# Kernel tuning notes

Hardware: AMD Instinct MI355X
Metric: run time of the kernel (lower is better)

The kernel has to match this reference:

```python
import jax, jax.numpy as jnp
import numpy as np

B, M, L, LQ, E, V = 32, 100, 30, 30, 256, 32000


def position_encoding(seq_len, emb):
    # faithful to MemN2N position encoding: 1 + 4*(k - (E+1)/2)*(j - (J+1)/2)/(E*J)
    j = jnp.arange(1, seq_len + 1, dtype=jnp.float32)[:, None]   # (J,1)
    k = jnp.arange(1, emb + 1, dtype=jnp.float32)[None, :]       # (1,E)
    half_e = (emb + 1) / 2.0
    half_j = (seq_len + 1) / 2.0
    return 1.0 + 4.0 * (k - half_e) * (j - half_j) / (emb * seq_len)  # (J,E)


def masked_softmax(x, m):
    xm = jnp.where(m > 0, x, -1e30)
    e = jnp.exp(xm - jnp.max(xm, axis=-1, keepdims=True)) * m
    return e / (jnp.sum(e, axis=-1, keepdims=True) + 1e-13)


def masked_log_softmax(x, m):
    return jax.nn.log_softmax(x + jnp.log(m + 1e-13), axis=-1)


def _forward(trainS, trainQ, trainVM, trainPM, trainSM, trainQM,
             A1, A2, A3, A4, W, b, gamma, beta):
    # query encoding: embed + position encode + query mask + sum over words
    Q = trainQ[:, 0, :]                                   # (B,LQ)
    pe_q = position_encoding(LQ, E)                       # (LQ,E)
    u = jnp.sum(A1[Q] * pe_q * trainQM[:, :, None], axis=1)  # (B,E)

    # story memory embeddings: gather + PE + sum over words.
    # NOTE: original code multiplies by trainSM but discards the result (bug),
    # so SM is intentionally NOT applied here.
    pe_s = position_encoding(L, E)                        # (L,E)
    embA1 = jnp.sum(A1[trainS] * pe_s, axis=2)            # (B,M,E)
    embA2 = jnp.sum(A2[trainS] * pe_s, axis=2)
    embA3 = jnp.sum(A3[trainS] * pe_s, axis=2)
    embA4 = jnp.sum(A4[trainS] * pe_s, axis=2)

    def hop(memA, memC, u):
        # scores = sum_E(memA * u) * PM (PM applied pre-sum is equivalent)
        scores = jnp.einsum('bme,be->bm', memA, u) * trainPM
        p = masked_softmax(scores, trainPM)               # (B,M)
        o = jnp.einsum('bm,bme->be', p, memC)             # (B,E)
        return o + u

    u = hop(embA1, embA2, u)   # hop 1
    u = hop(embA2, embA3, u)   # hop 2
    u = hop(embA3, embA4, u)   # hop 3

    # final linear + BatchNorm1d (training-mode batch stats, eps=1e-5)
    wx = u @ W.T + b                                      # (B,V)
    mean = jnp.mean(wx, axis=0)
    var = jnp.mean((wx - mean) ** 2, axis=0)
    y = gamma * (wx - mean) / jnp.sqrt(var + 1e-5) + beta
    return masked_log_softmax(y, trainVM)


def setup_inputs() -> dict:
    key = jax.random.key(0)
    ks = jax.random.split(key, 8)
    inp = {
        'trainS': jax.random.randint(ks[0], (B, M, L), 0, V, dtype=jnp.int32),
        'trainQ': jax.random.randint(ks[1], (B, 1, LQ), 0, V, dtype=jnp.int32),
        'trainVM': jnp.ones((B, V), jnp.float32),
        'trainPM': jnp.ones((B, M), jnp.float32),
        'trainSM': jnp.ones((B, M, L), jnp.float32),
        'trainQM': jnp.ones((B, LQ), jnp.float32),
        'A1': 0.1 * jax.random.normal(ks[2], (V, E), jnp.float32),
        'A2': 0.1 * jax.random.normal(ks[3], (V, E), jnp.float32),
        'A3': 0.1 * jax.random.normal(ks[4], (V, E), jnp.float32),
        'A4': 0.1 * jax.random.normal(ks[5], (V, E), jnp.float32),
        'W': jax.random.normal(ks[6], (V, E), jnp.float32) / np.sqrt(E),
        'b': jnp.zeros((V,), jnp.float32),
        'gamma': jnp.ones((V,), jnp.float32),
        'beta': jnp.zeros((V,), jnp.float32),
        'inspect': 0,
    }
    return inp


def reference(trainS, trainQ, trainVM, trainPM, trainSM, trainQM,
              A1, A2, A3, A4, W, b, gamma, beta, inspect):
    return _forward(trainS, trainQ, trainVM, trainPM, trainSM, trainQM,
                    A1, A2, A3, A4, W, b, gamma, beta)
```

## Files before the change

kernel.cpp:

```cpp
#include <hip/hip_runtime.h>
#include <math.h>

static constexpr int B_ = 32, M_ = 100, L_ = 30, LQ_ = 30, E_ = 256, V_ = 32000;

__global__ __launch_bounds__(256) void k_embed(const int* __restrict__ trainS,
                                               const float* __restrict__ A1,
                                               const float* __restrict__ A2,
                                               const float* __restrict__ A3,
                                               const float* __restrict__ A4,
                                               float* __restrict__ embA) {
    const int bm = blockIdx.x;
    const int tbl = threadIdx.x >> 6;
    const int e0 = (threadIdx.x & 63) * 4;
    const float* __restrict__ A = (tbl == 0) ? A1 : (tbl == 1) ? A2 : (tbl == 2) ? A3 : A4;
    const float half_e = (E_ + 1) * 0.5f;
    const float half_j = (L_ + 1) * 0.5f;
    const float inv = 1.0f / (float)(E_ * L_);
    const float k0 = (float)(e0 + 1) - half_e;
    const float k1 = k0 + 1.f, k2 = k0 + 2.f, k3 = k0 + 3.f;

    int idx[L_];
#pragma unroll
    for (int l = 0; l < L_; ++l) idx[l] = trainS[bm * L_ + l];

    float4 acc = make_float4(0.f, 0.f, 0.f, 0.f);
#pragma unroll
    for (int c = 0; c < 2; ++c) {
        float4 r[15];
#pragma unroll
        for (int j = 0; j < 15; ++j)
            r[j] = *reinterpret_cast<const float4*>(A + (size_t)idx[c * 15 + j] * E_ + e0);
        __builtin_amdgcn_sched_barrier(0);
#pragma unroll
        for (int j = 0; j < 15; ++j) {
            const int l = c * 15 + j;
            const float coef = 4.0f * ((float)(l + 1) - half_j) * inv;
            acc.x += r[j].x * (1.0f + coef * k0);
            acc.y += r[j].y * (1.0f + coef * k1);
            acc.z += r[j].z * (1.0f + coef * k2);
            acc.w += r[j].w * (1.0f + coef * k3);
        }
    }
    *reinterpret_cast<float4*>(embA + (size_t)tbl * (B_ * M_ * E_) + (size_t)bm * E_ + e0) = acc;
}

__global__ __launch_bounds__(1024) void k_hops(const int* __restrict__ trainQ,
                                               const float* __restrict__ trainQM,
                                               const float* __restrict__ A1,
                                               const float* __restrict__ embA,
                                               const float* __restrict__ trainPM,
                                               float* __restrict__ u_T,
                                               float* __restrict__ partial) {
    const int b = blockIdx.x;
    const int tid = threadIdx.x;
    const int lane = tid & 63;
    const int wave = tid >> 6;
    const int g = tid >> 8;
    const int e = tid & 255;
    if (tid == 0) partial[b] = 0.f;
    __shared__ float u_sh[E_];
    __shared__ float sc[M_];
    __shared__ float p_sh[M_];
    __shared__ float osum[4][E_];

    {
        const float half_e = (E_ + 1) * 0.5f;
        const float half_j = (LQ_ + 1) * 0.5f;
        const float inv = 1.0f / (float)(E_ * LQ_);
        const float ke = (float)(e + 1) - half_e;
        const int l0 = g * 8;
        const int ln = (LQ_ - l0 < 8) ? (LQ_ - l0) : 8;
        int qi[8];
        float qm[8];
#pragma unroll
        for (int j = 0; j < 8; ++j) {
            if (j < ln) {
                qi[j] = trainQ[b * LQ_ + l0 + j];
                qm[j] = trainQM[b * LQ_ + l0 + j];
            } else { qi[j] = 0; qm[j] = 0.f; }
        }
        float r[8];
#pragma unroll
        for (int j = 0; j < 8; ++j)
            r[j] = (j < ln) ? A1[(size_t)qi[j] * E_ + e] : 0.f;
        float part = 0.f;
#pragma unroll
        for (int j = 0; j < 8; ++j) {
            const float pe = 1.0f + 4.0f * ke * ((float)(l0 + j + 1) - half_j) * inv;
            part += r[j] * pe * qm[j];
        }
        osum[g][e] = part;
    }
    __syncthreads();
    if (tid < E_) u_sh[tid] = osum[0][tid] + osum[1][tid] + osum[2][tid] + osum[3][tid];
    __syncthreads();

    for (int hop = 0; hop < 3; ++hop) {
        const float* memA = embA + (size_t)hop * (B_ * M_ * E_) + (size_t)b * M_ * E_;
        const float* memC = memA + (size_t)(B_ * M_ * E_);
#pragma unroll 2
        for (int m = wave; m < M_; m += 16) {
            const float* row = memA + m * E_;
            float part = 0.f;
#pragma unroll
            for (int j = 0; j < 4; ++j)
                part += row[lane + 64 * j] * u_sh[lane + 64 * j];
#pragma unroll
            for (int off = 32; off > 0; off >>= 1)
                part += __shfl_xor(part, off, 64);
            if (lane == 0) sc[m] = part * trainPM[b * M_ + m];
        }
        __syncthreads();
        if (wave == 0) {
            const float pm0 = (lane < M_) ? trainPM[b * M_ + lane] : 0.f;
            const float pm1 = (lane + 64 < M_) ? trainPM[b * M_ + lane + 64] : 0.f;
            const float x0 = (lane < M_ && pm0 > 0.f) ? sc[lane] : -1e30f;
            const float x1 = (lane + 64 < M_ && pm1 > 0.f) ? sc[lane + 64] : -1e30f;
            float mx = fmaxf(x0, x1);
#pragma unroll
            for (int off = 32; off > 0; off >>= 1)
                mx = fmaxf(mx, __shfl_xor(mx, off, 64));
            const float e0v = (lane < M_) ? expf(x0 - mx) * pm0 : 0.f;
            const float e1v = (lane + 64 < M_) ? expf(x1 - mx) * pm1 : 0.f;
            float ssum = e0v + e1v;
#pragma unroll
            for (int off = 32; off > 0; off >>= 1)
                ssum += __shfl_xor(ssum, off, 64);
            const float invs = 1.0f / (ssum + 1e-13f);
            if (lane < M_) p_sh[lane] = e0v * invs;
            if (lane + 64 < M_) p_sh[lane + 64] = e1v * invs;
        }
        __syncthreads();
        {
            float acc = 0.f;
            const float* crow = memC + e;
            const int m0 = g * 25;
#pragma unroll 5
            for (int mm = 0; mm < 25; ++mm)
                acc += p_sh[m0 + mm] * crow[(size_t)(m0 + mm) * E_];
            osum[g][e] = acc;
        }
        __syncthreads();
        if (tid < E_) u_sh[tid] += osum[0][tid] + osum[1][tid] + osum[2][tid] + osum[3][tid];
        __syncthreads();
    }
    if (tid < E_) u_T[tid * B_ + b] = u_sh[tid];
}

__global__ __launch_bounds__(256) void k_output(const float* __restrict__ u_T,
                                                const float* __restrict__ Wm,
                                                const float* __restrict__ bias,
                                                const float* __restrict__ gamma,
                                                const float* __restrict__ beta,
                                                const float* __restrict__ VM,
                                                float* __restrict__ z,
                                                float* __restrict__ partial) {
    __shared__ float u_lds[E_ * B_];
    __shared__ float pex[B_];
    const int tid = threadIdx.x;
    for (int i = tid; i < (E_ * B_) / 4; i += 256)
        reinterpret_cast<float4*>(u_lds)[i] = reinterpret_cast<const float4*>(u_T)[i];
    if (tid < B_) pex[tid] = 0.f;
    __syncthreads();

    const int bg = tid & 7;
    const int vl = tid >> 3;
    const int v0 = blockIdx.x * 64 + vl * 2;
    const int v1 = v0 + 1;
    const float* __restrict__ wr0 = Wm + (size_t)v0 * E_;
    const float* __restrict__ wr1 = Wm + (size_t)v1 * E_;

    float accA[4] = {0.f, 0.f, 0.f, 0.f};
    float accB[4] = {0.f, 0.f, 0.f, 0.f};

#pragma unroll
    for (int c = 0; c < 8; ++c) {
        float4 wa[8], wb[8];
#pragma unroll
        for (int j = 0; j < 8; ++j) {
            wa[j] = reinterpret_cast<const float4*>(wr0)[c * 8 + j];
            wb[j] = reinterpret_cast<const float4*>(wr1)[c * 8 + j];
        }
        __builtin_amdgcn_sched_barrier(0);
#pragma unroll
        for (int j = 0; j < 8; ++j) {
#pragma unroll
            for (int eo = 0; eo < 4; ++eo) {
                const int e = c * 32 + j * 4 + eo;
                const float4 u4 = *reinterpret_cast<const float4*>(u_lds + e * B_ + bg * 4);
                const float w0 = (eo == 0) ? wa[j].x : (eo == 1) ? wa[j].y : (eo == 2) ? wa[j].z : wa[j].w;
                const float w1 = (eo == 0) ? wb[j].x : (eo == 1) ? wb[j].y : (eo == 2) ? wb[j].z : wb[j].w;
                accA[0] += w0 * u4.x; accA[1] += w0 * u4.y; accA[2] += w0 * u4.z; accA[3] += w0 * u4.w;
                accB[0] += w1 * u4.x; accB[1] += w1 * u4.y; accB[2] += w1 * u4.z; accB[3] += w1 * u4.w;
            }
        }
    }

    const float bvA = bias[v0], bvB = bias[v1];
    float s1a = 0.f, s2a = 0.f, s1b = 0.f, s2b = 0.f;
#pragma unroll
    for (int i = 0; i < 4; ++i) {
        accA[i] += bvA; accB[i] += bvB;
        s1a += accA[i]; s2a += accA[i] * accA[i];
        s1b += accB[i]; s2b += accB[i] * accB[i];
    }
#pragma unroll
    for (int off = 1; off < 8; off <<= 1) {
        s1a += __shfl_xor(s1a, off, 64);
        s2a += __shfl_xor(s2a, off, 64);
        s1b += __shfl_xor(s1b, off, 64);
        s2b += __shfl_xor(s2b, off, 64);
    }
    const float meanA = s1a * (1.0f / B_);
    const float meanB = s1b * (1.0f / B_);
    const float varA = s2a * (1.0f / B_) - meanA * meanA;
    const float varB = s2b * (1.0f / B_) - meanB * meanB;
    const float rstdA = rsqrtf(varA + 1e-5f);
    const float rstdB = rsqrtf(varB + 1e-5f);
    const float gA = gamma[v0], beA = beta[v0];
    const float gB = gamma[v1], beB = beta[v1];

    float exs[4];
#pragma unroll
    for (int i = 0; i < 4; ++i) {
        const int b = bg * 4 + i;
        const size_t row = (size_t)b * V_;
        const float vm0 = VM[row + v0] + 1e-13f;
        const float vm1 = VM[row + v1] + 1e-13f;
        const float y0 = gA * (accA[i] - meanA) * rstdA + beA;
        const float y1 = gB * (accB[i] - meanB) * rstdB + beB;
        z[row + v0] = y0 + logf(vm0);
        z[row + v1] = y1 + logf(vm1);
        exs[i] = vm0 * expf(y0) + vm1 * expf(y1);
    }
#pragma unroll
    for (int i = 0; i < 4; ++i)
        atomicAdd(&pex[bg * 4 + i], exs[i]);
    __syncthreads();
    if (tid < B_) atomicAdd(&partial[tid], pex[tid]);
}

__global__ __launch_bounds__(256) void k_final(const float* __restrict__ z,
                                               const float* __restrict__ partial,
                                               float* __restrict__ out) {
    const int idx = blockIdx.x * 256 + threadIdx.x;
    const int b = idx / (V_ / 4);
    const int v4 = idx % (V_ / 4);
    const float lse = logf(partial[b]);
    const float4 x = reinterpret_cast<const float4*>(z + (size_t)b * V_)[v4];
    float4 o;
    o.x = x.x - lse; o.y = x.y - lse; o.z = x.z - lse; o.w = x.w - lse;
    reinterpret_cast<float4*>(out + (size_t)b * V_)[v4] = o;
}

extern "C" void kernel_launch(void* const* d_in, const int* in_sizes, int n_in,
                              void* d_out, int out_size, void* d_ws, size_t ws_size,
                              hipStream_t stream) {
    const int* trainS = (const int*)d_in[0];
    const int* trainQ = (const int*)d_in[1];
    const float* trainVM = (const float*)d_in[2];
    const float* trainPM = (const float*)d_in[3];
    const float* trainQM = (const float*)d_in[5];
    const float* A1 = (const float*)d_in[6];
    const float* A2 = (const float*)d_in[7];
    const float* A3 = (const float*)d_in[8];
    const float* A4 = (const float*)d_in[9];
    const float* Wm = (const float*)d_in[10];
    const float* bias = (const float*)d_in[11];
    const float* gamma = (const float*)d_in[12];
    const float* beta = (const float*)d_in[13];
    float* out = (float*)d_out;

    float* ws = (float*)d_ws;
    float* u_T = ws;
    float* embA = ws + 8192;
    float* z = embA + 4 * (B_ * M_ * E_);
    float* partial = z + (size_t)B_ * V_;

    k_embed<<<B_ * M_, 256, 0, stream>>>(trainS, A1, A2, A3, A4, embA);
    k_hops<<<B_, 1024, 0, stream>>>(trainQ, trainQM, A1, embA, trainPM, u_T, partial);
    k_output<<<V_ / 64, 256, 0, stream>>>(u_T, Wm, bias, gamma, beta, trainVM, z, partial);
    k_final<<<(B_ * V_ / 4) / 256, 256, 0, stream>>>(z, partial, out);
}
```

Baseline: 107.0 us.

## Halve vocab rows per block, double-buffer W loads, shard softmax partial sums

The output GEMM kernel now gives each thread one vocab row instead of two and launches twice as many blocks. A non-unrolled loop double-buffers the W register loads so the next chunk is fetched while the current one is multiplied. The per-batch exp-sum accumulator is split into 8 slots indexed by block, which cuts global atomic contention, and the final kernel sums the slots. The intent is more parallelism and less register pressure, at the cost of more blocks each reloading the 32 KB u tile into LDS and halved reuse of each u value loaded from LDS.

```diff
diff --git a/kernel.cpp b/kernel.cpp
--- a/kernel.cpp
+++ b/kernel.cpp
@@ -57,7 +57,7 @@
     const int wave = tid >> 6;
     const int g = tid >> 8;
     const int e = tid & 255;
-    if (tid == 0) partial[b] = 0.f;
+    if (tid < 8) partial[b * 8 + tid] = 0.f;
     __shared__ float u_sh[E_];
     __shared__ float sc[M_];
     __shared__ float p_sh[M_];
@@ -165,79 +165,79 @@
 
     const int bg = tid & 7;
     const int vl = tid >> 3;
-    const int v0 = blockIdx.x * 64 + vl * 2;
-    const int v1 = v0 + 1;
-    const float* __restrict__ wr0 = Wm + (size_t)v0 * E_;
-    const float* __restrict__ wr1 = Wm + (size_t)v1 * E_;
-
-    float accA[4] = {0.f, 0.f, 0.f, 0.f};
-    float accB[4] = {0.f, 0.f, 0.f, 0.f};
-
-#pragma unroll
-    for (int c = 0; c < 8; ++c) {
-        float4 wa[8], wb[8];
-#pragma unroll
-        for (int j = 0; j < 8; ++j) {
-            wa[j] = reinterpret_cast<const float4*>(wr0)[c * 8 + j];
-            wb[j] = reinterpret_cast<const float4*>(wr1)[c * 8 + j];
-        }
-        __builtin_amdgcn_sched_barrier(0);
-#pragma unroll
-        for (int j = 0; j < 8; ++j) {
-#pragma unroll
-            for (int eo = 0; eo < 4; ++eo) {
-                const int e = c * 32 + j * 4 + eo;
-                const float4 u4 = *reinterpret_cast<const float4*>(u_lds + e * B_ + bg * 4);
-                const float w0 = (eo == 0) ? wa[j].x : (eo == 1) ? wa[j].y : (eo == 2) ? wa[j].z : wa[j].w;
-                const float w1 = (eo == 0) ? wb[j].x : (eo == 1) ? wb[j].y : (eo == 2) ? wb[j].z : wb[j].w;
-                accA[0] += w0 * u4.x; accA[1] += w0 * u4.y; accA[2] += w0 * u4.z; accA[3] += w0 * u4.w;
-                accB[0] += w1 * u4.x; accB[1] += w1 * u4.y; accB[2] += w1 * u4.z; accB[3] += w1 * u4.w;
+    const int v = blockIdx.x * 32 + vl;
+    const float* __restrict__ wr = Wm + (size_t)v * E_;
+
+    float acc[4] = {0.f, 0.f, 0.f, 0.f};
+    float4 wA[4], wB[4];
+#pragma unroll
+    for (int c = 0; c < 4; ++c) wA[c] = reinterpret_cast<const float4*>(wr)[c];
+
+#pragma unroll 1
+    for (int cc = 0; cc < 16; cc += 2) {
+#pragma unroll
+        for (int c = 0; c < 4; ++c) wB[c] = reinterpret_cast<const float4*>(wr)[(cc + 1) * 4 + c];
+#pragma unroll
+        for (int c = 0; c < 4; ++c) {
+#pragma unroll
+            for (int q = 0; q < 4; ++q) {
+                const int e = cc * 16 + c * 4 + q;
+                const float4 u4 = *reinterpret_cast<const float4*>(&u_lds[e * B_ + bg * 4]);
+                const float w = (q == 0) ? wA[c].x : (q == 1) ? wA[c].y : (q == 2) ? wA[c].z : wA[c].w;
+                acc[0] += w * u4.x; acc[1] += w * u4.y; acc[2] += w * u4.z; acc[3] += w * u4.w;
             }
         }
-    }
-
-    const float bvA = bias[v0], bvB = bias[v1];
-    float s1a = 0.f, s2a = 0.f, s1b = 0.f, s2b = 0.f;
+        if (cc + 2 < 16) {
+#pragma unroll
+            for (int c = 0; c < 4; ++c) wA[c] = reinterpret_cast<const float4*>(wr)[(cc + 2) * 4 + c];
+        }
+#pragma unroll
+        for (int c = 0; c < 4; ++c) {
+#pragma unroll
+            for (int q = 0; q < 4; ++q) {
+                const int e = (cc + 1) * 16 + c * 4 + q;
+                const float4 u4 = *reinterpret_cast<const float4*>(&u_lds[e * B_ + bg * 4]);
+                const float w = (q == 0) ? wB[c].x : (q == 1) ? wB[c].y : (q == 2) ? wB[c].z : wB[c].w;
+                acc[0] += w * u4.x; acc[1] += w * u4.y; acc[2] += w * u4.z; acc[3] += w * u4.w;
+            }
+        }
+    }
+
+    const float bv = bias[v];
+    float s1 = 0.f, s2 = 0.f;
 #pragma unroll
     for (int i = 0; i < 4; ++i) {
-        accA[i] += bvA; accB[i] += bvB;
-        s1a += accA[i]; s2a += accA[i] * accA[i];
-        s1b += accB[i]; s2b += accB[i] * accB[i];
+        acc[i] += bv;
+        s1 += acc[i];
+        s2 += acc[i] * acc[i];
     }
 #pragma unroll
     for (int off = 1; off < 8; off <<= 1) {
-        s1a += __shfl_xor(s1a, off, 64);
-        s2a += __shfl_xor(s2a, off, 64);
-        s1b += __shfl_xor(s1b, off, 64);
-        s2b += __shfl_xor(s2b, off, 64);
-    }
-    const float meanA = s1a * (1.0f / B_);
-    const float meanB = s1b * (1.0f / B_);
-    const float varA = s2a * (1.0f / B_) - meanA * meanA;
-    const float varB = s2b * (1.0f / B_) - meanB * meanB;
-    const float rstdA = rsqrtf(varA + 1e-5f);
-    const float rstdB = rsqrtf(varB + 1e-5f);
-    const float gA = gamma[v0], beA = beta[v0];
-    const float gB = gamma[v1], beB = beta[v1];
-
-    float exs[4];
+        s1 += __shfl_xor(s1, off, 64);
+        s2 += __shfl_xor(s2, off, 64);
+    }
+    const float mean = s1 * (1.0f / B_);
+    const float var = s2 * (1.0f / B_) - mean * mean;
+    const float rstd = rsqrtf(var + 1e-5f);
+    const float g = gamma[v], be = beta[v];
+
+    float exs = 0.f;
+    float ex[4];
 #pragma unroll
     for (int i = 0; i < 4; ++i) {
         const int b = bg * 4 + i;
-        const size_t row = (size_t)b * V_;
-        const float vm0 = VM[row + v0] + 1e-13f;
-        const float vm1 = VM[row + v1] + 1e-13f;
-        const float y0 = gA * (accA[i] - meanA) * rstdA + beA;
-        const float y1 = gB * (accB[i] - meanB) * rstdB + beB;
-        z[row + v0] = y0 + logf(vm0);
-        z[row + v1] = y1 + logf(vm1);
-        exs[i] = vm0 * expf(y0) + vm1 * expf(y1);
+        const size_t row = (size_t)b * V_ + v;
+        const float vm = VM[row] + 1e-13f;
+        const float y = g * (acc[i] - mean) * rstd + be;
+        z[row] = y + logf(vm);
+        ex[i] = vm * expf(y);
     }
 #pragma unroll
     for (int i = 0; i < 4; ++i)
-        atomicAdd(&pex[bg * 4 + i], exs[i]);
-    __syncthreads();
-    if (tid < B_) atomicAdd(&partial[tid], pex[tid]);
+        atomicAdd(&pex[bg * 4 + i], ex[i]);
+    (void)exs;
+    __syncthreads();
+    if (tid < B_) atomicAdd(&partial[tid * 8 + (blockIdx.x & 7)], pex[tid]);
 }
 
 __global__ __launch_bounds__(256) void k_final(const float* __restrict__ z,
@@ -246,7 +246,10 @@
     const int idx = blockIdx.x * 256 + threadIdx.x;
     const int b = idx / (V_ / 4);
     const int v4 = idx % (V_ / 4);
-    const float lse = logf(partial[b]);
+    float s = 0.f;
+#pragma unroll
+    for (int k = 0; k < 8; ++k) s += partial[b * 8 + k];
+    const float lse = logf(s);
     const float4 x = reinterpret_cast<const float4*>(z + (size_t)b * V_)[v4];
     float4 o;
     o.x = x.x - lse; o.y = x.y - lse; o.z = x.z - lse; o.w = x.w - lse;
@@ -279,6 +282,6 @@
 
     k_embed<<<B_ * M_, 256, 0, stream>>>(trainS, A1, A2, A3, A4, embA);
     k_hops<<<B_, 1024, 0, stream>>>(trainQ, trainQM, A1, embA, trainPM, u_T, partial);
-    k_output<<<V_ / 64, 256, 0, stream>>>(u_T, Wm, bias, gamma, beta, trainVM, z, partial);
+    k_output<<<V_ / 32, 256, 0, stream>>>(u_T, Wm, bias, gamma, beta, trainVM, z, partial);
     k_final<<<(B_ * V_ / 4) / 256, 256, 0, stream>>>(z, partial, out);
 }
```

Result: slower. 120.9 us (+13.0%).

## Double-buffer W row loads in output GEMV and shard partial-sum atomics

Applied to the files above, without the earlier changes.

Replaces the fully unrolled batched W load loop in k_output with a rolled loop that keeps two register buffers of W fragments. Each step loads the next fragments while computing on the current ones, aiming for software pipelining with lower register pressure. The per-batch exp-sum atomics are also spread across 8 slots selected by block index, which reduces contention on the 32 global addresses. k_final then sums the 8 slots, and the hop kernel zeroes all 8. The rolled loop may expose more load latency than the old fully unrolled version.

```diff
diff --git a/kernel.cpp b/kernel.cpp
--- a/kernel.cpp
+++ b/kernel.cpp
@@ -57,7 +57,7 @@
     const int wave = tid >> 6;
     const int g = tid >> 8;
     const int e = tid & 255;
-    if (tid == 0) partial[b] = 0.f;
+    if (tid < 8) partial[b * 8 + tid] = 0.f;
     __shared__ float u_sh[E_];
     __shared__ float sc[M_];
     __shared__ float p_sh[M_];
@@ -146,6 +146,27 @@
     }
     if (tid < E_) u_T[tid * B_ + b] = u_sh[tid];
 }
+
+#define COMPUTE8(W0A, W0B, W1A, W1B, EBASE)                                          \
+    {                                                                                \
+        _Pragma("unroll")                                                            \
+        for (int q = 0; q < 8; ++q) {                                                \
+            const float4 u4 = *reinterpret_cast<const float4*>(                      \
+                &u_lds[((EBASE) + q) * B_ + bg * 4]);                                \
+            const float w0 = (q < 4) ? ((q == 0) ? (W0A).x : (q == 1) ? (W0A).y      \
+                                        : (q == 2) ? (W0A).z : (W0A).w)              \
+                                     : ((q == 4) ? (W0B).x : (q == 5) ? (W0B).y      \
+                                        : (q == 6) ? (W0B).z : (W0B).w);             \
+            const float w1 = (q < 4) ? ((q == 0) ? (W1A).x : (q == 1) ? (W1A).y      \
+                                        : (q == 2) ? (W1A).z : (W1A).w)              \
+                                     : ((q == 4) ? (W1B).x : (q == 5) ? (W1B).y      \
+                                        : (q == 6) ? (W1B).z : (W1B).w);             \
+            acc0[0] += w0 * u4.x; acc0[1] += w0 * u4.y;                              \
+            acc0[2] += w0 * u4.z; acc0[3] += w0 * u4.w;                              \
+            acc1[0] += w1 * u4.x; acc1[1] += w1 * u4.y;                              \
+            acc1[2] += w1 * u4.z; acc1[3] += w1 * u4.w;                              \
+        }                                                                            \
+    }
 
 __global__ __launch_bounds__(256) void k_output(const float* __restrict__ u_T,
                                                 const float* __restrict__ Wm,
@@ -167,42 +188,33 @@
     const int vl = tid >> 3;
     const int v0 = blockIdx.x * 64 + vl * 2;
     const int v1 = v0 + 1;
-    const float* __restrict__ wr0 = Wm + (size_t)v0 * E_;
-    const float* __restrict__ wr1 = Wm + (size_t)v1 * E_;
-
-    float accA[4] = {0.f, 0.f, 0.f, 0.f};
-    float accB[4] = {0.f, 0.f, 0.f, 0.f};
-
-#pragma unroll
-    for (int c = 0; c < 8; ++c) {
-        float4 wa[8], wb[8];
-#pragma unroll
-        for (int j = 0; j < 8; ++j) {
-            wa[j] = reinterpret_cast<const float4*>(wr0)[c * 8 + j];
-            wb[j] = reinterpret_cast<const float4*>(wr1)[c * 8 + j];
-        }
-        __builtin_amdgcn_sched_barrier(0);
-#pragma unroll
-        for (int j = 0; j < 8; ++j) {
-#pragma unroll
-            for (int eo = 0; eo < 4; ++eo) {
-                const int e = c * 32 + j * 4 + eo;
-                const float4 u4 = *reinterpret_cast<const float4*>(u_lds + e * B_ + bg * 4);
-                const float w0 = (eo == 0) ? wa[j].x : (eo == 1) ? wa[j].y : (eo == 2) ? wa[j].z : wa[j].w;
-                const float w1 = (eo == 0) ? wb[j].x : (eo == 1) ? wb[j].y : (eo == 2) ? wb[j].z : wb[j].w;
-                accA[0] += w0 * u4.x; accA[1] += w0 * u4.y; accA[2] += w0 * u4.z; accA[3] += w0 * u4.w;
-                accB[0] += w1 * u4.x; accB[1] += w1 * u4.y; accB[2] += w1 * u4.z; accB[3] += w1 * u4.w;
-            }
-        }
-    }
-
-    const float bvA = bias[v0], bvB = bias[v1];
+    const float4* __restrict__ wp0 = reinterpret_cast<const float4*>(Wm + (size_t)v0 * E_);
+    const float4* __restrict__ wp1 = reinterpret_cast<const float4*>(Wm + (size_t)v1 * E_);
+
+    float acc0[4] = {0.f, 0.f, 0.f, 0.f};
+    float acc1[4] = {0.f, 0.f, 0.f, 0.f};
+
+    float4 A0a = wp0[0], A0b = wp0[1], A1a = wp1[0], A1b = wp1[1];
+    float4 B0a, B0b, B1a, B1b;
+#pragma unroll 1
+    for (int s = 0; s < 32; s += 2) {
+        B0a = wp0[(s + 1) * 2]; B0b = wp0[(s + 1) * 2 + 1];
+        B1a = wp1[(s + 1) * 2]; B1b = wp1[(s + 1) * 2 + 1];
+        COMPUTE8(A0a, A0b, A1a, A1b, s * 8);
+        if (s + 2 < 32) {
+            A0a = wp0[(s + 2) * 2]; A0b = wp0[(s + 2) * 2 + 1];
+            A1a = wp1[(s + 2) * 2]; A1b = wp1[(s + 2) * 2 + 1];
+        }
+        COMPUTE8(B0a, B0b, B1a, B1b, (s + 1) * 8);
+    }
+
+    const float bv0 = bias[v0], bv1 = bias[v1];
     float s1a = 0.f, s2a = 0.f, s1b = 0.f, s2b = 0.f;
 #pragma unroll
     for (int i = 0; i < 4; ++i) {
-        accA[i] += bvA; accB[i] += bvB;
-        s1a += accA[i]; s2a += accA[i] * accA[i];
-        s1b += accB[i]; s2b += accB[i] * accB[i];
+        acc0[i] += bv0; acc1[i] += bv1;
+        s1a += acc0[i]; s2a += acc0[i] * acc0[i];
+        s1b += acc1[i]; s2b += acc1[i] * acc1[i];
     }
 #pragma unroll
     for (int off = 1; off < 8; off <<= 1) {
@@ -220,24 +232,24 @@
     const float gA = gamma[v0], beA = beta[v0];
     const float gB = gamma[v1], beB = beta[v1];
 
-    float exs[4];
+    float ex[4];
 #pragma unroll
     for (int i = 0; i < 4; ++i) {
         const int b = bg * 4 + i;
         const size_t row = (size_t)b * V_;
         const float vm0 = VM[row + v0] + 1e-13f;
         const float vm1 = VM[row + v1] + 1e-13f;
-        const float y0 = gA * (accA[i] - meanA) * rstdA + beA;
-        const float y1 = gB * (accB[i] - meanB) * rstdB + beB;
+        const float y0 = gA * (acc0[i] - meanA) * rstdA + beA;
+        const float y1 = gB * (acc1[i] - meanB) * rstdB + beB;
         z[row + v0] = y0 + logf(vm0);
         z[row + v1] = y1 + logf(vm1);
-        exs[i] = vm0 * expf(y0) + vm1 * expf(y1);
+        ex[i] = vm0 * expf(y0) + vm1 * expf(y1);
     }
 #pragma unroll
     for (int i = 0; i < 4; ++i)
-        atomicAdd(&pex[bg * 4 + i], exs[i]);
-    __syncthreads();
-    if (tid < B_) atomicAdd(&partial[tid], pex[tid]);
+        atomicAdd(&pex[bg * 4 + i], ex[i]);
+    __syncthreads();
+    if (tid < B_) atomicAdd(&partial[tid * 8 + (blockIdx.x & 7)], pex[tid]);
 }
 
 __global__ __launch_bounds__(256) void k_final(const float* __restrict__ z,
@@ -246,7 +258,10 @@
     const int idx = blockIdx.x * 256 + threadIdx.x;
     const int b = idx / (V_ / 4);
     const int v4 = idx % (V_ / 4);
-    const float lse = logf(partial[b]);
+    float s = 0.f;
+#pragma unroll
+    for (int k = 0; k < 8; ++k) s += partial[b * 8 + k];
+    const float lse = logf(s);
     const float4 x = reinterpret_cast<const float4*>(z + (size_t)b * V_)[v4];
     float4 o;
     o.x = x.x - lse; o.y = x.y - lse; o.z = x.z - lse; o.w = x.w - lse;
```

After: 115.3 us. +7.8%, slower.
